# Kernel optimization log

Hardware: AMD Instinct MI355X
Metric: run time of the kernel (lower is better)

## Reference

```python
import jax, jax.numpy as jnp
from jax import lax
import numpy as np

N_STEPS = 21

def _conv3x3(a, w):
    # NCHW input, OIHW weight, stride 1, padding 1 ('same' for 3x3)
    return lax.conv_general_dilated(
        a, w, window_strides=(1, 1), padding=[(1, 1), (1, 1)],
        dimension_numbers=('NCHW', 'OIHW', 'NCHW'))

def setup_inputs() -> dict:
    key = jax.random.key(0)
    x = jax.random.normal(key, (32, 1, 1024, 1024), dtype=jnp.float32)
    convAx = jnp.array([[[[0.2538, 0.5022, 0.07344],
                          [0.17864, 1.0622, 0.24616],
                          [0.2454, 0.90548, 0.52616]]]], dtype=jnp.float32)
    convBx = jnp.array([[[[-0.083, -3.15852, 3.24172],
                          [-2.0894, -9.34624, -2.0018],
                          [6.889, -1.53384, 7.71856]]]], dtype=jnp.float32)
    biasx = jnp.array([-0.07002], dtype=jnp.float32)
    return {"x": x, "convAx": convAx, "convBx": convBx, "biasx": biasx}

def reference(x, convAx, convBx, biasx):
    # global min-max normalization to [-1, 1]
    xmin = jnp.min(x)
    xmax = jnp.max(x)
    xn = (x - xmin) * (2.0 / (xmax - xmin)) - 1.0
    # fixed drive term
    BU = _conv3x3(xn, convBx)  # [B,1,H,W]
    bias = biasx.reshape(1, -1, 1, 1)
    s0 = jnp.zeros_like(xn)

    def step(s, _):
        s = _conv3x3(s, convAx) + bias + BU
        s = jnp.clip(s, -1.0, 1.0)  # activeFun = hard clamp to [-1,1]
        return s, None

    s, _ = lax.scan(step, s0, None, length=N_STEPS)
    return (s + 1.0) * 0.5
```

## Files before the change

### kernel.cpp

```cpp
#include <hip/hip_runtime.h>

#define HW 1024
#define NIMG 32
#define IMGPX ((size_t)HW * HW)
#define NELEM (NIMG * IMGPX)

typedef float f2 __attribute__((ext_vector_type(2)));

#define RING 6
#define TOX 116
#define TOY 52
#define NBX 9
#define NBY 20
#define LSTR 136
#define SLOTS 34
#define BUFW (SLOTS * LSTR)

__device__ __forceinline__ unsigned f2su(float f) {
    unsigned u = __float_as_uint(f);
    return (u & 0x80000000u) ? ~u : (u | 0x80000000u);
}
__device__ __forceinline__ float s2f(unsigned u) {
    return __uint_as_float((u & 0x80000000u) ? (u & 0x7fffffffu) : ~u);
}

__global__ void mm_init(unsigned* mm) {
    mm[0] = 0xFFFFFFFFu;
    mm[1] = 0u;
}

__global__ __launch_bounds__(256) void mm_reduce(const float4* __restrict__ x,
                                                 unsigned* mm, int n4) {
    const int tid = threadIdx.x;
    int gid = blockIdx.x * blockDim.x + tid;
    const int stride = gridDim.x * blockDim.x;
    float vmin = 3.4e38f, vmax = -3.4e38f;
    for (int i = gid; i < n4; i += stride) {
        float4 v = x[i];
        vmin = fminf(vmin, fminf(fminf(v.x, v.y), fminf(v.z, v.w)));
        vmax = fmaxf(vmax, fmaxf(fmaxf(v.x, v.y), fmaxf(v.z, v.w)));
    }
    __shared__ float smin[256];
    __shared__ float smax[256];
    smin[tid] = vmin; smax[tid] = vmax;
    __syncthreads();
    for (int s = 128; s > 0; s >>= 1) {
        if (tid < s) {
            smin[tid] = fminf(smin[tid], smin[tid + s]);
            smax[tid] = fmaxf(smax[tid], smax[tid + s]);
        }
        __syncthreads();
    }
    if (tid == 0) {
        atomicMin(&mm[0], f2su(smin[0]));
        atomicMax(&mm[1], f2su(smax[0]));
    }
}

struct RowW { f2 P[2]; float L, R; };

template <int FIRST, int LAST>
__global__ __launch_bounds__(512) void fused_k(
    const float* __restrict__ x, const float* __restrict__ sin_,
    float* __restrict__ sout, const unsigned* __restrict__ mm,
    const float* __restrict__ wAp, const float* __restrict__ wBp,
    const float* __restrict__ biasp) {
#pragma clang fp contract(off)
    __shared__ float sb[2 * BUFW];
    const int tid = threadIdx.x;
    const int tx = tid & 31;
    const int tyg = tid >> 5;
    const int lane = tid & 63;
    const int laneL = (lane + 63) & 63;
    const int laneR = (lane + 1) & 63;
    const int r0 = tyg << 2;
    const int c0 = tx << 2;
    const int bx = (int)blockIdx.x, by = (int)blockIdx.y;
    const int ox = bx * TOX - RING;
    const int oy = by * TOY - RING;
    const size_t img = (size_t)blockIdx.z * IMGPX;
    const bool edgeX = (bx == 0) | (bx == NBX - 1);
    const bool edgeY = (by == 0) | (by == NBY - 1);
    const bool intr = !(edgeX | edgeY);

    const float xmin = s2f(mm[0]);
    const float xmax = s2f(mm[1]);
    const float scale = 2.0f / (xmax - xmin);
    const float b = biasp[0];

    auto ldSlot = [&](int wb) -> RowW {
        RowW o;
        const float4 q0 = *reinterpret_cast<const float4*>(&sb[wb + c0]);
        o.P[0] = f2{q0.x, q0.y}; o.P[1] = f2{q0.z, q0.w};
        const float fromL = __shfl(q0.w, laneL);
        const float fromR = __shfl(q0.x, laneR);
        o.L = (tx == 0) ? sb[wb + 130] : fromL;
        o.R = (tx == 31) ? sb[wb + 131] : fromR;
        return o;
    };

    float cf[9];
    auto conv9 = [&](const RowW& A, const RowW& B, const RowW& C, int p) -> f2 {
#pragma clang fp contract(off)
        f2 acc = f2{0.0f, 0.0f};
        f2 tl, tr;
        tl = f2{(p == 0) ? A.L : A.P[0].y, A.P[p].x};
        tr = f2{A.P[p].y, (p == 0) ? A.P[1].x : A.R};
        acc = acc + f2{cf[0], cf[0]} * tl;
        acc = acc + f2{cf[1], cf[1]} * A.P[p];
        acc = acc + f2{cf[2], cf[2]} * tr;
        tl = f2{(p == 0) ? B.L : B.P[0].y, B.P[p].x};
        tr = f2{B.P[p].y, (p == 0) ? B.P[1].x : B.R};
        acc = acc + f2{cf[3], cf[3]} * tl;
        acc = acc + f2{cf[4], cf[4]} * B.P[p];
        acc = acc + f2{cf[5], cf[5]} * tr;
        tl = f2{(p == 0) ? C.L : C.P[0].y, C.P[p].x};
        tr = f2{C.P[p].y, (p == 0) ? C.P[1].x : C.R};
        acc = acc + f2{cf[6], cf[6]} * tl;
        acc = acc + f2{cf[7], cf[7]} * C.P[p];
        acc = acc + f2{cf[8], cf[8]} * tr;
        return acc;
    };

    if (intr) {
        for (int k = tid; k < 66 * 130; k += 512) {
            const int si = k / 130;
            const int cc = (k - si * 130) - 1;
            const int w = (cc == -1) ? 130 : ((cc == 128) ? 131 : cc);
            const float v =
                (x[img + (size_t)(oy + si - 1) * HW + (ox + cc)] - xmin) * scale - 1.0f;
            sb[si * LSTR + w] = v;
        }
    } else {
        for (int k = tid; k < 66 * 130; k += 512) {
            const int si = k / 130;
            const int cc = (k - si * 130) - 1;
            const int w = (cc == -1) ? 130 : ((cc == 128) ? 131 : cc);
            const int gr = oy + si - 1;
            const int gc = ox + cc;
            float v = 0.0f;
            if (gr >= 0 && gr < HW && gc >= 0 && gc < HW)
                v = (x[img + (size_t)gr * HW + gc] - xmin) * scale - 1.0f;
            sb[si * LSTR + w] = v;
        }
    }
    __syncthreads();

#pragma unroll
    for (int i = 0; i < 9; ++i) cf[i] = wBp[i];
    f2 bu[4][2];
    {
        RowW prev = ldSlot((r0) * LSTR);
        RowW cur = ldSlot((r0 + 1) * LSTR);
#pragma unroll
        for (int i = 0; i < 4; ++i) {
            RowW nxt = ldSlot((r0 + 2 + i) * LSTR);
            bu[i][0] = conv9(prev, cur, nxt, 0);
            bu[i][1] = conv9(prev, cur, nxt, 1);
            prev = cur; cur = nxt;
        }
    }
    __syncthreads();

    f2 res[4][2];
    float hS[4];
    for (int k = tid; k < 324; k += 512) {
        int rr, cc;
        if (k < 260) { rr = (k < 130) ? -1 : 64; cc = (k % 130) - 1; }
        else {
            const int kk = k - 260;
            const int s = kk >> 1;
            rr = (s & 1) ? ((s >> 1) * 4 + 3) : ((s >> 1) * 4);
            cc = (kk & 1) ? 128 : -1;
        }
        const int w = (cc == -1) ? 130 : ((cc == 128) ? 131 : cc);
        const int slot = (rr == -1) ? 0 : ((rr == 64) ? 33 : ((rr >> 2) * 2 + 1 + (((rr & 3) == 3) ? 1 : 0)));
        float v = 0.0f;
        if (!FIRST) {
            const int gr = oy + rr, gc = ox + cc;
            if (gr >= 0 && gr < HW && gc >= 0 && gc < HW)
                v = sin_[img + (size_t)gr * HW + gc];
        }
        const int wo = slot * LSTR + w;
        sb[wo] = v;
        sb[BUFW + wo] = v;
    }
    if (FIRST) {
#pragma unroll
        for (int i = 0; i < 4; ++i) {
            hS[i] = 0.0f;
            res[i][0] = f2{0.0f, 0.0f};
            res[i][1] = f2{0.0f, 0.0f};
        }
    } else if (intr) {
#pragma unroll
        for (int i = 0; i < 4; ++i) {
            const float2* src = reinterpret_cast<const float2*>(
                &sin_[img + (size_t)(oy + r0 + i) * HW + ox + c0]);
            const float2 t0 = src[0];
            const float2 t1 = src[1];
            res[i][0] = f2{t0.x, t0.y};
            res[i][1] = f2{t1.x, t1.y};
            float hv = 0.0f;
            if (tx == 0) hv = sin_[img + (size_t)(oy + r0 + i) * HW + (ox - 1)];
            else if (tx == 31) hv = sin_[img + (size_t)(oy + r0 + i) * HW + (ox + 128)];
            hS[i] = hv;
        }
    } else {
#pragma unroll
        for (int i = 0; i < 4; ++i) {
            const int gr = oy + r0 + i;
            const bool rin = (gr >= 0) & (gr < HW);
#pragma unroll
            for (int cl = 0; cl < 4; ++cl) {
                const int gc = ox + c0 + cl;
                float v = 0.0f;
                if (rin && gc >= 0 && gc < HW) v = sin_[img + (size_t)gr * HW + gc];
                res[i][cl >> 1][cl & 1] = v;
            }
            float hv = 0.0f;
            if (tx == 0) {
                const int gc = ox - 1;
                if (rin && gc >= 0) hv = sin_[img + (size_t)gr * HW + gc];
            } else if (tx == 31) {
                const int gc = ox + 128;
                if (rin && gc < HW) hv = sin_[img + (size_t)gr * HW + gc];
            }
            hS[i] = hv;
        }
    }

    auto wrRow = [&](int bo, int i, int slot) {
        *reinterpret_cast<float4*>(&sb[bo + slot * LSTR + c0]) =
            make_float4(res[i][0].x, res[i][0].y, res[i][1].x, res[i][1].y);
    };
    wrRow(0, 0, 2 * tyg + 1);
    wrRow(0, 3, 2 * tyg + 2);
    __syncthreads();

#pragma unroll
    for (int i = 0; i < 9; ++i) cf[i] = wAp[i];
    float mR[4];
#pragma unroll
    for (int i = 0; i < 4; ++i) {
        const int g = oy + r0 + i;
        mR[i] = (g >= 0 && g < HW) ? 1.0f : 0.0f;
    }
    f2 mC2[2];
#pragma unroll
    for (int p = 0; p < 2; ++p) {
        const int g0 = ox + c0 + 2 * p, g1 = g0 + 1;
        mC2[p] = f2{(g0 >= 0 && g0 < HW) ? 1.0f : 0.0f,
                    (g1 >= 0 && g1 < HW) ? 1.0f : 0.0f};
    }

    auto buildRow = [&](const f2 pr[2], float hs) -> RowW {
        RowW o;
        o.P[0] = pr[0]; o.P[1] = pr[1];
        const float fromL = __shfl(pr[1].y, laneL);
        const float fromR = __shfl(pr[0].x, laneR);
        o.L = (tx == 0) ? hs : fromL;
        o.R = (tx == 31) ? hs : fromR;
        return o;
    };

    const int slotM1 = (tyg == 0) ? 0 : 2 * tyg;
    const int slotP4 = (tyg == 15) ? 33 : 2 * tyg + 3;

#pragma unroll 1
    for (int t = 0; t < 7; ++t) {
        const int rdo = (t & 1) * BUFW;
        const int wro = BUFW - rdo;
        RowW prev = ldSlot(rdo + slotM1 * LSTR);
        RowW cur = buildRow(res[0], hS[0]);
#pragma unroll
        for (int i = 0; i < 4; ++i) {
            RowW nxt = (i < 3) ? buildRow(res[i + 1], hS[i + 1])
                               : ldSlot(rdo + slotP4 * LSTR);
            f2 n0 = conv9(prev, cur, nxt, 0);
            f2 n1 = conv9(prev, cur, nxt, 1);
            n0 = (n0 + f2{b, b}) + bu[i][0];
            n1 = (n1 + f2{b, b}) + bu[i][1];
            n0 = __builtin_elementwise_max(n0, f2{-1.0f, -1.0f});
            n0 = __builtin_elementwise_min(n0, f2{1.0f, 1.0f});
            n1 = __builtin_elementwise_max(n1, f2{-1.0f, -1.0f});
            n1 = __builtin_elementwise_min(n1, f2{1.0f, 1.0f});
            if (!intr) {
                n0 = n0 * f2{mR[i], mR[i]};
                n1 = n1 * f2{mR[i], mR[i]};
                n0 = n0 * mC2[0];
                n1 = n1 * mC2[1];
            }
            prev = cur; cur = nxt;
            res[i][0] = n0; res[i][1] = n1;
        }
        wrRow(wro, 0, 2 * tyg + 1);
        wrRow(wro, 3, 2 * tyg + 2);
        __syncthreads();
    }

    const bool fullc = intr && (c0 >= RING) && (c0 + 3 < RING + TOX);
#pragma unroll
    for (int i = 0; i < 4; ++i) {
        const int r = r0 + i;
        if (r < RING || r >= RING + TOY) continue;
        const int gr = oy + r;
        if (gr >= HW) continue;
        if (fullc) {
            float2* dst = reinterpret_cast<float2*>(&sout[img + (size_t)gr * HW + ox + c0]);
            f2 v0 = res[i][0], v1 = res[i][1];
            if (LAST) {
                v0 = (v0 + f2{1.0f, 1.0f}) * f2{0.5f, 0.5f};
                v1 = (v1 + f2{1.0f, 1.0f}) * f2{0.5f, 0.5f};
            }
            dst[0] = make_float2(v0.x, v0.y);
            dst[1] = make_float2(v1.x, v1.y);
        } else {
#pragma unroll
            for (int cl = 0; cl < 4; ++cl) {
                const int c = c0 + cl;
                if (c < RING || c >= RING + TOX) continue;
                const int gc = ox + c;
                if (gc < 0 || gc >= HW) continue;
                float v = res[i][cl >> 1][cl & 1];
                if (LAST) v = (v + 1.0f) * 0.5f;
                sout[img + (size_t)gr * HW + gc] = v;
            }
        }
    }
}

extern "C" void kernel_launch(void* const* d_in, const int* in_sizes, int n_in,
                              void* d_out, int out_size, void* d_ws, size_t ws_size,
                              hipStream_t stream) {
    const float* x = (const float*)d_in[0];
    const float* wA = (const float*)d_in[1];
    const float* wB = (const float*)d_in[2];
    const float* bias = (const float*)d_in[3];
    float* out = (float*)d_out;
    unsigned* mm = (unsigned*)d_ws;
    float* pong = (float*)((char*)d_ws + 1024);

    mm_init<<<1, 1, 0, stream>>>(mm);
    mm_reduce<<<2048, 256, 0, stream>>>((const float4*)x, mm, (int)(NELEM / 4));

    dim3 grid(NBX, NBY, NIMG);
    fused_k<1, 0><<<grid, 512, 0, stream>>>(x, nullptr, out, mm, wA, wB, bias);
    fused_k<0, 0><<<grid, 512, 0, stream>>>(x, out, pong, mm, wA, wB, bias);
    fused_k<0, 1><<<grid, 512, 0, stream>>>(x, pong, out, mm, wA, wB, bias);
}
```

Measured before the change: 796.6 us.

## Use 256-thread blocks with 8 rows per thread and halved LDS halo buffer

```diff
diff --git a/kernel.cpp b/kernel.cpp
--- a/kernel.cpp
+++ b/kernel.cpp
@@ -13,7 +13,7 @@
 #define NBX 9
 #define NBY 20
 #define LSTR 136
-#define SLOTS 34
+#define SLOTS 18
 #define BUFW (SLOTS * LSTR)
 
 __device__ __forceinline__ unsigned f2su(float f) {
@@ -60,7 +60,7 @@
 struct RowW { f2 P[2]; float L, R; };
 
 template <int FIRST, int LAST>
-__global__ __launch_bounds__(512) void fused_k(
+__global__ __launch_bounds__(256) void fused_k(
     const float* __restrict__ x, const float* __restrict__ sin_,
     float* __restrict__ sout, const unsigned* __restrict__ mm,
     const float* __restrict__ wAp, const float* __restrict__ wBp,
@@ -73,7 +73,7 @@
     const int lane = tid & 63;
     const int laneL = (lane + 63) & 63;
     const int laneR = (lane + 1) & 63;
-    const int r0 = tyg << 2;
+    const int r0 = tyg << 3;
     const int c0 = tx << 2;
     const int bx = (int)blockIdx.x, by = (int)blockIdx.y;
     const int ox = bx * TOX - RING;
@@ -122,59 +122,79 @@
         return acc;
     };
 
-    if (intr) {
-        for (int k = tid; k < 66 * 130; k += 512) {
-            const int si = k / 130;
-            const int cc = (k - si * 130) - 1;
-            const int w = (cc == -1) ? 130 : ((cc == 128) ? 131 : cc);
-            const float v =
-                (x[img + (size_t)(oy + si - 1) * HW + (ox + cc)] - xmin) * scale - 1.0f;
-            sb[si * LSTR + w] = v;
-        }
-    } else {
-        for (int k = tid; k < 66 * 130; k += 512) {
-            const int si = k / 130;
-            const int cc = (k - si * 130) - 1;
-            const int w = (cc == -1) ? 130 : ((cc == 128) ? 131 : cc);
-            const int gr = oy + si - 1;
-            const int gc = ox + cc;
-            float v = 0.0f;
-            if (gr >= 0 && gr < HW && gc >= 0 && gc < HW)
-                v = (x[img + (size_t)gr * HW + gc] - xmin) * scale - 1.0f;
-            sb[si * LSTR + w] = v;
-        }
-    }
-    __syncthreads();
+    auto stageXn = [&](int row0s) {
+        if (intr) {
+            for (int k = tid; k < 34 * 130; k += 256) {
+                const int si = k / 130;
+                const int cc = (k - si * 130) - 1;
+                const int w = (cc == -1) ? 130 : ((cc == 128) ? 131 : cc);
+                const float v =
+                    (x[img + (size_t)(oy + row0s + si) * HW + (ox + cc)] - xmin) * scale - 1.0f;
+                sb[si * LSTR + w] = v;
+            }
+        } else {
+            for (int k = tid; k < 34 * 130; k += 256) {
+                const int si = k / 130;
+                const int cc = (k - si * 130) - 1;
+                const int w = (cc == -1) ? 130 : ((cc == 128) ? 131 : cc);
+                const int gr = oy + row0s + si;
+                const int gc = ox + cc;
+                float v = 0.0f;
+                if (gr >= 0 && gr < HW && gc >= 0 && gc < HW)
+                    v = (x[img + (size_t)gr * HW + gc] - xmin) * scale - 1.0f;
+                sb[si * LSTR + w] = v;
+            }
+        }
+    };
 
 #pragma unroll
     for (int i = 0; i < 9; ++i) cf[i] = wBp[i];
-    f2 bu[4][2];
+    f2 bu[8][2];
     {
-        RowW prev = ldSlot((r0) * LSTR);
-        RowW cur = ldSlot((r0 + 1) * LSTR);
-#pragma unroll
-        for (int i = 0; i < 4; ++i) {
-            RowW nxt = ldSlot((r0 + 2 + i) * LSTR);
-            bu[i][0] = conv9(prev, cur, nxt, 0);
-            bu[i][1] = conv9(prev, cur, nxt, 1);
-            prev = cur; cur = nxt;
-        }
-    }
-    __syncthreads();
-
-    f2 res[4][2];
-    float hS[4];
-    for (int k = tid; k < 324; k += 512) {
+        stageXn(-1);
+        __syncthreads();
+        if (tyg < 4) {
+            RowW prev = ldSlot((r0) * LSTR);
+            RowW cur = ldSlot((r0 + 1) * LSTR);
+#pragma unroll
+            for (int i = 0; i < 8; ++i) {
+                RowW nxt = ldSlot((r0 + 2 + i) * LSTR);
+                bu[i][0] = conv9(prev, cur, nxt, 0);
+                bu[i][1] = conv9(prev, cur, nxt, 1);
+                prev = cur; cur = nxt;
+            }
+        }
+        __syncthreads();
+        stageXn(31);
+        __syncthreads();
+        if (tyg >= 4) {
+            const int s0 = r0 - 32;
+            RowW prev = ldSlot((s0) * LSTR);
+            RowW cur = ldSlot((s0 + 1) * LSTR);
+#pragma unroll
+            for (int i = 0; i < 8; ++i) {
+                RowW nxt = ldSlot((s0 + 2 + i) * LSTR);
+                bu[i][0] = conv9(prev, cur, nxt, 0);
+                bu[i][1] = conv9(prev, cur, nxt, 1);
+                prev = cur; cur = nxt;
+            }
+        }
+        __syncthreads();
+    }
+
+    f2 res[8][2];
+    float hS[8];
+    for (int k = tid; k < 292; k += 256) {
         int rr, cc;
         if (k < 260) { rr = (k < 130) ? -1 : 64; cc = (k % 130) - 1; }
         else {
             const int kk = k - 260;
             const int s = kk >> 1;
-            rr = (s & 1) ? ((s >> 1) * 4 + 3) : ((s >> 1) * 4);
+            rr = (s & 1) ? ((s >> 1) * 8 + 7) : ((s >> 1) * 8);
             cc = (kk & 1) ? 128 : -1;
         }
         const int w = (cc == -1) ? 130 : ((cc == 128) ? 131 : cc);
-        const int slot = (rr == -1) ? 0 : ((rr == 64) ? 33 : ((rr >> 2) * 2 + 1 + (((rr & 3) == 3) ? 1 : 0)));
+        const int slot = (rr == -1) ? 0 : ((rr == 64) ? 17 : ((rr >> 3) * 2 + 1 + (((rr & 7) == 7) ? 1 : 0)));
         float v = 0.0f;
         if (!FIRST) {
             const int gr = oy + rr, gc = ox + cc;
@@ -187,14 +207,14 @@
     }
     if (FIRST) {
 #pragma unroll
-        for (int i = 0; i < 4; ++i) {
+        for (int i = 0; i < 8; ++i) {
             hS[i] = 0.0f;
             res[i][0] = f2{0.0f, 0.0f};
             res[i][1] = f2{0.0f, 0.0f};
         }
     } else if (intr) {
 #pragma unroll
-        for (int i = 0; i < 4; ++i) {
+        for (int i = 0; i < 8; ++i) {
             const float2* src = reinterpret_cast<const float2*>(
                 &sin_[img + (size_t)(oy + r0 + i) * HW + ox + c0]);
             const float2 t0 = src[0];
@@ -208,7 +228,7 @@
         }
     } else {
 #pragma unroll
-        for (int i = 0; i < 4; ++i) {
+        for (int i = 0; i < 8; ++i) {
             const int gr = oy + r0 + i;
             const bool rin = (gr >= 0) & (gr < HW);
 #pragma unroll
@@ -235,17 +255,11 @@
             make_float4(res[i][0].x, res[i][0].y, res[i][1].x, res[i][1].y);
     };
     wrRow(0, 0, 2 * tyg + 1);
-    wrRow(0, 3, 2 * tyg + 2);
+    wrRow(0, 7, 2 * tyg + 2);
     __syncthreads();
 
 #pragma unroll
     for (int i = 0; i < 9; ++i) cf[i] = wAp[i];
-    float mR[4];
-#pragma unroll
-    for (int i = 0; i < 4; ++i) {
-        const int g = oy + r0 + i;
-        mR[i] = (g >= 0 && g < HW) ? 1.0f : 0.0f;
-    }
     f2 mC2[2];
 #pragma unroll
     for (int p = 0; p < 2; ++p) {
@@ -265,7 +279,7 @@
     };
 
     const int slotM1 = (tyg == 0) ? 0 : 2 * tyg;
-    const int slotP4 = (tyg == 15) ? 33 : 2 * tyg + 3;
+    const int slotP8 = (tyg == 7) ? 17 : 2 * tyg + 3;
 
 #pragma unroll 1
     for (int t = 0; t < 7; ++t) {
@@ -274,9 +288,9 @@
         RowW prev = ldSlot(rdo + slotM1 * LSTR);
         RowW cur = buildRow(res[0], hS[0]);
 #pragma unroll
-        for (int i = 0; i < 4; ++i) {
-            RowW nxt = (i < 3) ? buildRow(res[i + 1], hS[i + 1])
-                               : ldSlot(rdo + slotP4 * LSTR);
+        for (int i = 0; i < 8; ++i) {
+            RowW nxt = (i < 7) ? buildRow(res[i + 1], hS[i + 1])
+                               : ldSlot(rdo + slotP8 * LSTR);
             f2 n0 = conv9(prev, cur, nxt, 0);
             f2 n1 = conv9(prev, cur, nxt, 1);
             n0 = (n0 + f2{b, b}) + bu[i][0];
@@ -286,8 +300,10 @@
             n1 = __builtin_elementwise_max(n1, f2{-1.0f, -1.0f});
             n1 = __builtin_elementwise_min(n1, f2{1.0f, 1.0f});
             if (!intr) {
-                n0 = n0 * f2{mR[i], mR[i]};
-                n1 = n1 * f2{mR[i], mR[i]};
+                const int gr = oy + r0 + i;
+                const float m = (gr >= 0 && gr < HW) ? 1.0f : 0.0f;
+                n0 = n0 * f2{m, m};
+                n1 = n1 * f2{m, m};
                 n0 = n0 * mC2[0];
                 n1 = n1 * mC2[1];
             }
@@ -295,13 +311,13 @@
             res[i][0] = n0; res[i][1] = n1;
         }
         wrRow(wro, 0, 2 * tyg + 1);
-        wrRow(wro, 3, 2 * tyg + 2);
+        wrRow(wro, 7, 2 * tyg + 2);
         __syncthreads();
     }
 
     const bool fullc = intr && (c0 >= RING) && (c0 + 3 < RING + TOX);
 #pragma unroll
-    for (int i = 0; i < 4; ++i) {
+    for (int i = 0; i < 8; ++i) {
         const int r = r0 + i;
         if (r < RING || r >= RING + TOY) continue;
         const int gr = oy + r;
@@ -345,7 +361,7 @@
     mm_reduce<<<2048, 256, 0, stream>>>((const float4*)x, mm, (int)(NELEM / 4));
 
     dim3 grid(NBX, NBY, NIMG);
-    fused_k<1, 0><<<grid, 512, 0, stream>>>(x, nullptr, out, mm, wA, wB, bias);
-    fused_k<0, 0><<<grid, 512, 0, stream>>>(x, out, pong, mm, wA, wB, bias);
-    fused_k<0, 1><<<grid, 512, 0, stream>>>(x, pong, out, mm, wA, wB, bias);
-}
+    fused_k<1, 0><<<grid, 256, 0, stream>>>(x, nullptr, out, mm, wA, wB, bias);
+    fused_k<0, 0><<<grid, 256, 0, stream>>>(x, out, pong, mm, wA, wB, bias);
+    fused_k<0, 1><<<grid, 256, 0, stream>>>(x, pong, out, mm, wA, wB, bias);
+}
```

Result: slower. 863.0 us (+8.3%).
